# Performance work log

Hardware: AMD Instinct MI355X
Metric: run time of the kernel (lower is better)

Reference implementation:

```python
import jax, jax.numpy as jnp
import numpy as np

N = 300000; E = N - 1; A = 150000; D = 64; H = 128; T = 512
NEG_SLOPE = 0.2


def _gatv2(h, src, dst, Wl, bl, Wr, br, att, bias):
    # PyG GATv2Conv, heads=1, add_self_loops=False
    xl = h @ Wl + bl            # source transform [N,H]
    xr = h @ Wr + br            # target transform [N,H]
    e = xl[src] + xr[dst]       # [E,H]
    a = jax.nn.leaky_relu(e, NEG_SLOPE) @ att   # [E]
    amax = jax.ops.segment_max(a, dst, num_segments=N)
    ex = jnp.exp(a - amax[dst])
    denom = jax.ops.segment_sum(ex, dst, num_segments=N)
    alpha = ex / (denom[dst] + 1e-16)
    out = jax.ops.segment_sum(alpha[:, None] * xl[src], dst, num_segments=N)
    return out + bias


def setup_inputs() -> dict:
    ks = jax.random.split(jax.random.key(0), 32)
    s = 0.02
    inp = {
        'x': jax.random.normal(ks[0], (N, D), jnp.float32),
        'edge_index': jax.random.randint(ks[1], (2, E), 0, N),
        'focal_seq': jax.random.normal(ks[2], (1, D), jnp.float32),
        'child_idx': jax.random.randint(ks[3], (A,), 0, N),
        'parent_idx': jax.random.randint(ks[4], (A,), 0, N + 1) - 1,  # include -1 (no parent)
        'time_idx': jax.random.randint(ks[5], (A,), 0, T),
        'W_embed': jax.random.normal(ks[6], (D, H)) * s, 'b_embed': jnp.zeros((H,)),
        'bu_Wl': jax.random.normal(ks[7], (H, H)) * s, 'bu_bl': jnp.zeros((H,)),
        'bu_Wr': jax.random.normal(ks[8], (H, H)) * s, 'bu_br': jnp.zeros((H,)),
        'bu_att': jax.random.normal(ks[9], (H,)) * s, 'bu_bias': jnp.zeros((H,)),
        'td_Wl': jax.random.normal(ks[10], (H, H)) * s, 'td_bl': jnp.zeros((H,)),
        'td_Wr': jax.random.normal(ks[11], (H, H)) * s, 'td_br': jnp.zeros((H,)),
        'td_att': jax.random.normal(ks[12], (H,)) * s, 'td_bias': jnp.zeros((H,)),
        'time_table': jax.random.normal(ks[13], (T, H)) * s,
        'W_comb': jax.random.normal(ks[14], (2 * H, H)) * s, 'b_comb': jnp.zeros((H,)),
        'W_a1': jax.random.normal(ks[15], (3 * H, H)) * s, 'b_a1': jnp.zeros((H,)),
        'W_a2': jax.random.normal(ks[16], (H, 1)) * s, 'b_a2': jnp.zeros((1,)),
        'W_seq': jax.random.normal(ks[17], (D, H)) * s, 'b_seq': jnp.zeros((H,)),
    }
    return inp


def reference(x, edge_index, focal_seq, child_idx, parent_idx, time_idx,
              W_embed, b_embed,
              bu_Wl, bu_bl, bu_Wr, bu_br, bu_att, bu_bias,
              td_Wl, td_bl, td_Wr, td_br, td_att, td_bias,
              time_table, W_comb, b_comb, W_a1, b_a1, W_a2, b_a2,
              W_seq, b_seq):
    h = x @ W_embed + b_embed                       # [N,H]
    # bottom-up pass: edge_index flipped -> src=row1, dst=row0
    h_bu = _gatv2(h, edge_index[1], edge_index[0], bu_Wl, bu_bl, bu_Wr, bu_br, bu_att, bu_bias)
    h = h + jax.nn.relu(h_bu)
    # top-down pass: src=row0, dst=row1
    h_td = _gatv2(h, edge_index[0], edge_index[1], td_Wl, td_bl, td_Wr, td_br, td_att, td_bias)
    h = h + jax.nn.relu(h_td)
    context = focal_seq @ W_seq + b_seq             # [1,H]
    h_child = h[child_idx]                          # [A,H]
    h_parent = jnp.where((parent_idx == -1)[:, None], 0.0, h[parent_idx])
    branch = jnp.concatenate([h_child, h_parent], axis=-1) @ W_comb + b_comb  # [A,H]
    t_emb = time_table[time_idx]                    # [A,H]
    combined = jnp.concatenate([branch, t_emb, jnp.broadcast_to(context, (branch.shape[0], context.shape[1]))], axis=-1)  # [A,3H]
    logits = jax.nn.relu(combined @ W_a1 + b_a1) @ W_a2 + b_a2  # [A,1]
    return logits
```

## Files before the change

### kernel.cpp

```cpp
#include <hip/hip_runtime.h>
#include <hip/hip_bf16.h>

#define NN 300000
#define EE 299999
#define AA 150000
#define DD 64
#define HH 128
#define TT 512
#define SCAN_NB ((NN + 1023) / 1024)

typedef unsigned short u16;
typedef unsigned int u32;
typedef __attribute__((ext_vector_type(8))) short short8;
typedef __attribute__((ext_vector_type(4))) float f32x4;

__device__ __forceinline__ float bfb(u16 u) { return __uint_as_float(((u32)u) << 16); }
__device__ __forceinline__ u16 f2b(float f) {
    u32 u = __float_as_uint(f);
    u32 r = (u + 0x7FFFu + ((u >> 16) & 1u)) >> 16;
    return (u16)r;
}
__device__ __forceinline__ uint4 load8(const u16* p) { return *(const uint4*)p; }
__device__ __forceinline__ uint4 load8(const float* p) {
    float4 f1 = *(const float4*)p;
    float4 f2 = *(const float4*)(p + 4);
    union { ushort s[8]; uint4 v; } u;
    u.s[0] = f2b(f1.x); u.s[1] = f2b(f1.y); u.s[2] = f2b(f1.z); u.s[3] = f2b(f1.w);
    u.s[4] = f2b(f2.x); u.s[5] = f2b(f2.y); u.s[6] = f2b(f2.z); u.s[7] = f2b(f2.w);
    return u.v;
}
__device__ __forceinline__ void unpack8(uint4 v, float* f) {
    u32 w0 = v.x, w1 = v.y, w2 = v.z, w3 = v.w;
    f[0] = bfb((u16)w0); f[1] = bfb((u16)(w0 >> 16));
    f[2] = bfb((u16)w1); f[3] = bfb((u16)(w1 >> 16));
    f[4] = bfb((u16)w2); f[5] = bfb((u16)(w2 >> 16));
    f[6] = bfb((u16)w3); f[7] = bfb((u16)(w3 >> 16));
}
__device__ __forceinline__ int swo(int row, int kblock) {
    return row * 64 + ((kblock ^ (row & 7)) * 8);
}

__global__ __launch_bounds__(256) void k_wtrans(const float* w0, const float* w1,
                                                const float* w2, const float* w3,
                                                const float* w4, const float* w5,
                                                const float* w6, const float* w7,
                                                u16* __restrict__ wt) {
    int widx = blockIdx.x >> 3, part = blockIdx.x & 7;
    const float* W; int K = 128;
    switch (widx) {
        case 0: W = w0; break; case 1: W = w1; break;
        case 2: W = w2; break; case 3: W = w3; break;
        case 4: W = w4; break; case 5: W = w5; break;
        case 6: W = w6; break; default: W = w7; K = 64; break;
    }
    u16* dst = wt + widx * 16384;
    int total = K * 128;
    int lo = part * 2048, hi = lo + 2048;
    if (hi > total) hi = total;
    for (int idx = lo + threadIdx.x; idx < hi; idx += 256) {
        int k = idx >> 7, n = idx & 127;
        dst[n * K + k] = f2b(W[k * 128 + n]);
    }
}

__global__ void k_context(const float* __restrict__ focal, const float* __restrict__ Wseq,
                          const float* __restrict__ bseq, float* __restrict__ ctx) {
    int t = threadIdx.x;
    float acc = bseq[t];
    for (int d = 0; d < DD; ++d) acc = fmaf(focal[d], Wseq[d * HH + t], acc);
    ctx[t] = acc;
}

__global__ void k_c1(const float* __restrict__ ctx, const float* __restrict__ Wa1c,
                     const float* __restrict__ ba1, float* __restrict__ c1) {
    int t = threadIdx.x;
    float acc = ba1[t];
    for (int k = 0; k < HH; ++k) acc = fmaf(ctx[k], Wa1c[k * HH + t], acc);
    c1[t] = acc;
}

__global__ void k_tproj(const float* __restrict__ tt, const float* __restrict__ Wa1m,
                        float* __restrict__ tproj) {
    int ti = blockIdx.x, t = threadIdx.x;
    float acc = 0.f;
    for (int k = 0; k < HH; ++k)
        acc = fmaf(tt[ti * HH + k], Wa1m[k * HH + t], acc);
    tproj[(size_t)ti * HH + t] = acc;
}

__global__ void k_hist(const int* __restrict__ dst, int* __restrict__ counts) {
    int e = blockIdx.x * 256 + threadIdx.x;
    if (e < EE) atomicAdd(&counts[dst[e]], 1);
}

__global__ __launch_bounds__(256) void k_scan_block(const int* __restrict__ in,
                                                    int* __restrict__ out,
                                                    int* __restrict__ bsum, int n) {
    __shared__ int sh[256];
    int b = blockIdx.x, t = threadIdx.x;
    int base = b * 1024 + t * 4;
    int v0 = (base + 0 < n) ? in[base + 0] : 0;
    int v1 = (base + 1 < n) ? in[base + 1] : 0;
    int v2 = (base + 2 < n) ? in[base + 2] : 0;
    int v3 = (base + 3 < n) ? in[base + 3] : 0;
    int tsum = v0 + v1 + v2 + v3;
    sh[t] = tsum;
    __syncthreads();
    for (int d = 1; d < 256; d <<= 1) {
        int x = (t >= d) ? sh[t - d] : 0;
        __syncthreads();
        sh[t] += x;
        __syncthreads();
    }
    int excl = sh[t] - tsum;
    if (t == 255) bsum[b] = sh[255];
    if (base + 0 < n) out[base + 0] = excl;
    if (base + 1 < n) out[base + 1] = excl + v0;
    if (base + 2 < n) out[base + 2] = excl + v0 + v1;
    if (base + 3 < n) out[base + 3] = excl + v0 + v1 + v2;
}

__global__ __launch_bounds__(256) void k_scan_top(int* __restrict__ data, int n) {
    __shared__ int sh[256];
    int t = threadIdx.x;
    int base = t * 4;
    int v0 = (base + 0 < n) ? data[base + 0] : 0;
    int v1 = (base + 1 < n) ? data[base + 1] : 0;
    int v2 = (base + 2 < n) ? data[base + 2] : 0;
    int v3 = (base + 3 < n) ? data[base + 3] : 0;
    int tsum = v0 + v1 + v2 + v3;
    sh[t] = tsum;
    __syncthreads();
    for (int d = 1; d < 256; d <<= 1) {
        int x = (t >= d) ? sh[t - d] : 0;
        __syncthreads();
        sh[t] += x;
        __syncthreads();
    }
    int excl = sh[t] - tsum;
    if (base + 0 < n) data[base + 0] = excl;
    if (base + 1 < n) data[base + 1] = excl + v0;
    if (base + 2 < n) data[base + 2] = excl + v0 + v1;
    if (base + 3 < n) data[base + 3] = excl + v0 + v1 + v2;
}

__global__ void k_scan_add(int* __restrict__ out, const int* __restrict__ bsum, int n) {
    int i = blockIdx.x * 256 + threadIdx.x;
    if (i < n) out[i] += bsum[i >> 10];
}

__global__ void k_settail(int* o1, int* o2) {
    if (threadIdx.x == 0) { o1[NN] = EE; o2[NN] = EE; }
}

__global__ void k_scatter(const int* __restrict__ src, const int* __restrict__ dst,
                          int* __restrict__ cursor, int* __restrict__ elist) {
    int e = blockIdx.x * 256 + threadIdx.x;
    if (e >= EE) return;
    int pos = atomicAdd(&cursor[dst[e]], 1);
    elist[pos] = src[e];
}

template <int K, typename InT>
__global__ __launch_bounds__(256) void k_mfma_proj(const InT* __restrict__ in,
                                                   const u16* __restrict__ WT,
                                                   const float* __restrict__ bias,
                                                   u16* __restrict__ out, int nrows) {
    __shared__ u16 lds[17408];
    u16* a_lds = lds;
    u16* b_lds = lds + 8192;
    u16* clds = lds;
    const int t = threadIdx.x;
    const int tile_m = blockIdx.x * 128;
    const int wave = t >> 6, l = t & 15, quad = (t >> 4) & 3;
    const int wr = wave >> 1, wc = wave & 1;
    f32x4 acc[4][4] = {};

    for (int chunk = 0; chunk < K / 64; ++chunk) {
        const int c0 = chunk * 64;
        __syncthreads();
        for (int ci = t; ci < 1024; ci += 256) {
            int row = ci >> 3, kc = ci & 7;
            int grow = tile_m + row;
            uint4 v = make_uint4(0, 0, 0, 0);
            if (grow < nrows) v = load8(&in[(size_t)grow * K + c0 + kc * 8]);
            *(uint4*)&a_lds[swo(row, kc)] = v;
        }
        for (int ci = t; ci < 1024; ci += 256) {
            int n = ci >> 3, kc = ci & 7;
            *(uint4*)&b_lds[swo(n, kc)] = *(const uint4*)&WT[(size_t)n * K + c0 + kc * 8];
        }
        __syncthreads();
#pragma unroll
        for (int ks = 0; ks < 2; ++ks) {
            short8 af[4], bf[4];
#pragma unroll
            for (int i = 0; i < 4; ++i)
                af[i] = *(const short8*)&a_lds[swo(wr * 64 + i * 16 + l, ks * 4 + quad)];
#pragma unroll
            for (int j = 0; j < 4; ++j)
                bf[j] = *(const short8*)&b_lds[swo(wc * 64 + j * 16 + l, ks * 4 + quad)];
#pragma unroll
            for (int i = 0; i < 4; ++i)
#pragma unroll
                for (int j = 0; j < 4; ++j)
                    acc[i][j] = __builtin_amdgcn_mfma_f32_16x16x32_bf16(af[i], bf[j], acc[i][j], 0, 0, 0);
        }
    }
    __syncthreads();
#pragma unroll
    for (int j = 0; j < 4; ++j) {
        int col = wc * 64 + j * 16 + l;
        float b = bias[col];
#pragma unroll
        for (int i = 0; i < 4; ++i) {
            int rloc = wr * 64 + i * 16 + quad * 4;
#pragma unroll
            for (int r = 0; r < 4; ++r)
                clds[(rloc + r) * 136 + col] = f2b(acc[i][j][r] + b);
        }
    }
    __syncthreads();
#pragma unroll
    for (int it = 0; it < 8; ++it) {
        int idx = it * 256 + t;
        int row = idx >> 4, c16 = idx & 15;
        int grow = tile_m + row;
        if (grow < nrows)
            *(uint4*)&out[(size_t)grow * HH + c16 * 8] = *(const uint4*)&clds[row * 136 + c16 * 8];
    }
}

__global__ __launch_bounds__(256) void k_mfma_proj2(const u16* __restrict__ in,
                                                    const u16* __restrict__ WT1,
                                                    const u16* __restrict__ WT2,
                                                    const float* __restrict__ b1,
                                                    const float* __restrict__ b2,
                                                    u16* __restrict__ out1,
                                                    u16* __restrict__ out2, int nrows) {
    __shared__ u16 lds[24576];
    u16* a_lds = lds;
    u16* b1_lds = lds + 8192;
    u16* b2_lds = lds + 16384;
    u16* clds = lds;
    const int t = threadIdx.x;
    const int tile_m = blockIdx.x * 128;
    const int wave = t >> 6, l = t & 15, quad = (t >> 4) & 3;
    const int wr = wave >> 1, wc = wave & 1;
    f32x4 acc1[4][4] = {}, acc2[4][4] = {};

    for (int chunk = 0; chunk < 2; ++chunk) {
        const int c0 = chunk * 64;
        __syncthreads();
        for (int ci = t; ci < 1024; ci += 256) {
            int row = ci >> 3, kc = ci & 7;
            int grow = tile_m + row;
            uint4 v = make_uint4(0, 0, 0, 0);
            if (grow < nrows) v = load8(&in[(size_t)grow * HH + c0 + kc * 8]);
            *(uint4*)&a_lds[swo(row, kc)] = v;
        }
        for (int ci = t; ci < 1024; ci += 256) {
            int n = ci >> 3, kc = ci & 7;
            *(uint4*)&b1_lds[swo(n, kc)] = *(const uint4*)&WT1[(size_t)n * HH + c0 + kc * 8];
            *(uint4*)&b2_lds[swo(n, kc)] = *(const uint4*)&WT2[(size_t)n * HH + c0 + kc * 8];
        }
        __syncthreads();
#pragma unroll
        for (int ks = 0; ks < 2; ++ks) {
            short8 af[4], bf1[4], bf2[4];
#pragma unroll
            for (int i = 0; i < 4; ++i)
                af[i] = *(const short8*)&a_lds[swo(wr * 64 + i * 16 + l, ks * 4 + quad)];
#pragma unroll
            for (int j = 0; j < 4; ++j) {
                bf1[j] = *(const short8*)&b1_lds[swo(wc * 64 + j * 16 + l, ks * 4 + quad)];
                bf2[j] = *(const short8*)&b2_lds[swo(wc * 64 + j * 16 + l, ks * 4 + quad)];
            }
#pragma unroll
            for (int i = 0; i < 4; ++i)
#pragma unroll
                for (int j = 0; j < 4; ++j) {
                    acc1[i][j] = __builtin_amdgcn_mfma_f32_16x16x32_bf16(af[i], bf1[j], acc1[i][j], 0, 0, 0);
                    acc2[i][j] = __builtin_amdgcn_mfma_f32_16x16x32_bf16(af[i], bf2[j], acc2[i][j], 0, 0, 0);
                }
        }
    }
    __syncthreads();
#pragma unroll
    for (int j = 0; j < 4; ++j) {
        int col = wc * 64 + j * 16 + l;
        float b = b1[col];
#pragma unroll
        for (int i = 0; i < 4; ++i) {
            int rloc = wr * 64 + i * 16 + quad * 4;
#pragma unroll
            for (int r = 0; r < 4; ++r)
                clds[(rloc + r) * 136 + col] = f2b(acc1[i][j][r] + b);
        }
    }
    __syncthreads();
#pragma unroll
    for (int it = 0; it < 8; ++it) {
        int idx = it * 256 + t;
        int row = idx >> 4, c16 = idx & 15;
        int grow = tile_m + row;
        if (grow < nrows)
            *(uint4*)&out1[(size_t)grow * HH + c16 * 8] = *(const uint4*)&clds[row * 136 + c16 * 8];
    }
    __syncthreads();
#pragma unroll
    for (int j = 0; j < 4; ++j) {
        int col = wc * 64 + j * 16 + l;
        float b = b2[col];
#pragma unroll
        for (int i = 0; i < 4; ++i) {
            int rloc = wr * 64 + i * 16 + quad * 4;
#pragma unroll
            for (int r = 0; r < 4; ++r)
                clds[(rloc + r) * 136 + col] = f2b(acc2[i][j][r] + b);
        }
    }
    __syncthreads();
#pragma unroll
    for (int it = 0; it < 8; ++it) {
        int idx = it * 256 + t;
        int row = idx >> 4, c16 = idx & 15;
        int grow = tile_m + row;
        if (grow < nrows)
            *(uint4*)&out2[(size_t)grow * HH + c16 * 8] = *(const uint4*)&clds[row * 136 + c16 * 8];
    }
}

__global__ __launch_bounds__(256) void k_mfma_gproj(const u16* __restrict__ h,
                                                    const int* __restrict__ idx1,
                                                    const int* __restrict__ idx2,
                                                    const u16* __restrict__ WT1,
                                                    const u16* __restrict__ WT2,
                                                    const float* __restrict__ bias,
                                                    u16* __restrict__ out, int nrows) {
    __shared__ u16 lds[17408];
    u16* a_lds = lds;
    u16* b_lds = lds + 8192;
    u16* clds = lds;
    const int t = threadIdx.x;
    const int tile_m = blockIdx.x * 128;
    const int wave = t >> 6, l = t & 15, quad = (t >> 4) & 3;
    const int wr = wave >> 1, wc = wave & 1;
    f32x4 acc[4][4] = {};

    for (int pass = 0; pass < 2; ++pass) {
        const int* idx = pass ? idx2 : idx1;
        const u16* WT = pass ? WT2 : WT1;
        for (int chunk = 0; chunk < 2; ++chunk) {
            const int c0 = chunk * 64;
            __syncthreads();
            for (int ci = t; ci < 1024; ci += 256) {
                int row = ci >> 3, kc = ci & 7;
                int item = tile_m + row;
                int g = (item < nrows) ? idx[item] : -1;
                uint4 v = make_uint4(0, 0, 0, 0);
                if (g >= 0) v = load8(&h[(size_t)g * HH + c0 + kc * 8]);
                *(uint4*)&a_lds[swo(row, kc)] = v;
            }
            for (int ci = t; ci < 1024; ci += 256) {
                int n = ci >> 3, kc = ci & 7;
                *(uint4*)&b_lds[swo(n, kc)] = *(const uint4*)&WT[(size_t)n * HH + c0 + kc * 8];
            }
            __syncthreads();
#pragma unroll
            for (int ks = 0; ks < 2; ++ks) {
                short8 af[4], bf[4];
#pragma unroll
                for (int i = 0; i < 4; ++i)
                    af[i] = *(const short8*)&a_lds[swo(wr * 64 + i * 16 + l, ks * 4 + quad)];
#pragma unroll
                for (int j = 0; j < 4; ++j)
                    bf[j] = *(const short8*)&b_lds[swo(wc * 64 + j * 16 + l, ks * 4 + quad)];
#pragma unroll
                for (int i = 0; i < 4; ++i)
#pragma unroll
                    for (int j = 0; j < 4; ++j)
                        acc[i][j] = __builtin_amdgcn_mfma_f32_16x16x32_bf16(af[i], bf[j], acc[i][j], 0, 0, 0);
            }
        }
    }
    __syncthreads();
#pragma unroll
    for (int j = 0; j < 4; ++j) {
        int col = wc * 64 + j * 16 + l;
        float b = bias[col];
#pragma unroll
        for (int i = 0; i < 4; ++i) {
            int rloc = wr * 64 + i * 16 + quad * 4;
#pragma unroll
            for (int r = 0; r < 4; ++r)
                clds[(rloc + r) * 136 + col] = f2b(acc[i][j][r] + b);
        }
    }
    __syncthreads();
#pragma unroll
    for (int it = 0; it < 8; ++it) {
        int idx = it * 256 + t;
        int row = idx >> 4, c16 = idx & 15;
        int item = tile_m + row;
        if (item < nrows)
            *(uint4*)&out[(size_t)item * HH + c16 * 8] = *(const uint4*)&clds[row * 136 + c16 * 8];
    }
}

__global__ __launch_bounds__(256) void k_mfma_zlogit(const u16* __restrict__ branch,
                                                     const int* __restrict__ time_idx,
                                                     const float* __restrict__ tproj,
                                                     const float* __restrict__ c1,
                                                     const u16* __restrict__ WTa1,
                                                     const float* __restrict__ Wa2,
                                                     const float* __restrict__ ba2,
                                                     float* __restrict__ out) {
    __shared__ u16 lds[16384];
    u16* a_lds = lds;
    u16* b_lds = lds + 8192;
    __shared__ float red[2][128];
    const int t = threadIdx.x;
    const int tile_m = blockIdx.x * 128;
    const int wave = t >> 6, l = t & 15, quad = (t >> 4) & 3;
    const int wr = wave >> 1, wc = wave & 1;
    f32x4 acc[4][4] = {};

    for (int chunk = 0; chunk < 2; ++chunk) {
        const int c0 = chunk * 64;
        __syncthreads();
        for (int ci = t; ci < 1024; ci += 256) {
            int row = ci >> 3, kc = ci & 7;
            int item = tile_m + row;
            uint4 v = make_uint4(0, 0, 0, 0);
            if (item < AA) v = load8(&branch[(size_t)item * HH + c0 + kc * 8]);
            *(uint4*)&a_lds[swo(row, kc)] = v;
        }
        for (int ci = t; ci < 1024; ci += 256) {
            int n = ci >> 3, kc = ci & 7;
            *(uint4*)&b_lds[swo(n, kc)] = *(const uint4*)&WTa1[(size_t)n * HH + c0 + kc * 8];
        }
        __syncthreads();
#pragma unroll
        for (int ks = 0; ks < 2; ++ks) {
            short8 af[4], bf[4];
#pragma unroll
            for (int i = 0; i < 4; ++i)
                af[i] = *(const short8*)&a_lds[swo(wr * 64 + i * 16 + l, ks * 4 + quad)];
#pragma unroll
            for (int j = 0; j < 4; ++j)
                bf[j] = *(const short8*)&b_lds[swo(wc * 64 + j * 16 + l, ks * 4 + quad)];
#pragma unroll
            for (int i = 0; i < 4; ++i)
#pragma unroll
                for (int j = 0; j < 4; ++j)
                    acc[i][j] = __builtin_amdgcn_mfma_f32_16x16x32_bf16(af[i], bf[j], acc[i][j], 0, 0, 0);
        }
    }
    float c1v[4], wa2v[4];
#pragma unroll
    for (int j = 0; j < 4; ++j) {
        int col = wc * 64 + j * 16 + l;
        c1v[j] = c1[col];
        wa2v[j] = Wa2[col];
    }
#pragma unroll
    for (int i = 0; i < 4; ++i) {
        int rbase = tile_m + wr * 64 + i * 16 + quad * 4;
#pragma unroll
        for (int r = 0; r < 4; ++r) {
            int item = rbase + r;
            int ti = (item < AA) ? time_idx[item] : 0;
            const float* tp = tproj + (size_t)ti * HH;
            float partial = 0.f;
#pragma unroll
            for (int j = 0; j < 4; ++j) {
                int col = wc * 64 + j * 16 + l;
                float z = fmaxf(acc[i][j][r] + tp[col] + c1v[j], 0.f);
                partial = fmaf(z, wa2v[j], partial);
            }
            partial += __shfl_xor(partial, 1);
            partial += __shfl_xor(partial, 2);
            partial += __shfl_xor(partial, 4);
            partial += __shfl_xor(partial, 8);
            if (l == 0) red[wc][wr * 64 + i * 16 + quad * 4 + r] = partial;
        }
    }
    __syncthreads();
    if (t < 128) {
        int item = tile_m + t;
        if (item < AA) out[item] = red[0][t] + red[1][t] + ba2[0];
    }
}

__global__ __launch_bounds__(256) void k_gat_fused(u16* __restrict__ h,
                                                   const u16* __restrict__ xl,
                                                   const u16* __restrict__ xr,
                                                   const int* __restrict__ offs,
                                                   const int* __restrict__ elist,
                                                   const float* __restrict__ att,
                                                   const float* __restrict__ bias) {
    int g = blockIdx.x * 16 + (threadIdx.x >> 4);
    int l = threadIdx.x & 15;
    float attv[8], biasv[8];
    *(float4*)&attv[0] = *(const float4*)&att[l * 8];
    *(float4*)&attv[4] = *(const float4*)&att[l * 8 + 4];
    *(float4*)&biasv[0] = *(const float4*)&bias[l * 8];
    *(float4*)&biasv[4] = *(const float4*)&bias[l * 8 + 4];
    float xrf[8];
    unpack8(*(const uint4*)&xr[(size_t)g * HH + l * 8], xrf);
    int e0 = offs[g], e1 = offs[g + 1];

    float m = -__builtin_inff(), s = 0.f;
    float acc[8] = {};
    for (int e = e0; e < e1; ++e) {
        int sidx = elist[e];
        float xf[8];
        unpack8(*(const uint4*)&xl[(size_t)sidx * HH + l * 8], xf);
        float p = 0.f;
#pragma unroll
        for (int j = 0; j < 8; ++j) {
            float v = xf[j] + xrf[j];
            v = v >= 0.f ? v : 0.2f * v;
            p = fmaf(v, attv[j], p);
        }
        p += __shfl_xor(p, 1); p += __shfl_xor(p, 2);
        p += __shfl_xor(p, 4); p += __shfl_xor(p, 8);
        float mn = fmaxf(m, p);
        float so = __expf(m - mn);
        float w = __expf(p - mn);
        s = s * so + w;
#pragma unroll
        for (int j = 0; j < 8; ++j) acc[j] = fmaf(acc[j], so, w * xf[j]);
        m = mn;
    }
    float inv = 1.f / (s + 1e-16f);

    float hf[8];
    unpack8(*(const uint4*)&h[(size_t)g * HH + l * 8], hf);
    union { ushort sh[8]; uint4 v; } o;
#pragma unroll
    for (int j = 0; j < 8; ++j) {
        hf[j] += fmaxf(fmaf(acc[j], inv, biasv[j]), 0.f);
        o.sh[j] = f2b(hf[j]);
    }
    *(uint4*)&h[(size_t)g * HH + l * 8] = o.v;
}

typedef const float* fp;

static void build_csr(const int* src, const int* dst, int* offs, int* elist,
                      int* work, int* bsum, hipStream_t stream) {
    hipMemsetAsync(work, 0, (size_t)NN * 4, stream);
    k_hist<<<(EE + 255) / 256, 256, 0, stream>>>(dst, work);
    k_scan_block<<<SCAN_NB, 256, 0, stream>>>(work, offs, bsum, NN);
    k_scan_top<<<1, 256, 0, stream>>>(bsum, SCAN_NB);
    k_scan_add<<<(NN + 255) / 256, 256, 0, stream>>>(offs, bsum, NN);
    hipMemcpyAsync(work, offs, (size_t)NN * 4, hipMemcpyDeviceToDevice, stream);
    k_scatter<<<(EE + 255) / 256, 256, 0, stream>>>(src, dst, work, elist);
}

extern "C" void kernel_launch(void* const* d_in, const int* in_sizes, int n_in,
                              void* d_out, int out_size, void* d_ws, size_t ws_size,
                              hipStream_t stream) {
    fp x                 = (fp)d_in[0];
    const int* ei        = (const int*)d_in[1];
    fp focal             = (fp)d_in[2];
    const int* child_idx = (const int*)d_in[3];
    const int* parent_idx= (const int*)d_in[4];
    const int* time_idx  = (const int*)d_in[5];
    fp W_embed = (fp)d_in[6],  b_embed = (fp)d_in[7];
    fp bu_Wl   = (fp)d_in[8],  bu_bl   = (fp)d_in[9];
    fp bu_Wr   = (fp)d_in[10], bu_br   = (fp)d_in[11];
    fp bu_att  = (fp)d_in[12], bu_bias = (fp)d_in[13];
    fp td_Wl   = (fp)d_in[14], td_bl   = (fp)d_in[15];
    fp td_Wr   = (fp)d_in[16], td_br   = (fp)d_in[17];
    fp td_att  = (fp)d_in[18], td_bias = (fp)d_in[19];
    fp time_table = (fp)d_in[20];
    fp W_comb  = (fp)d_in[21], b_comb  = (fp)d_in[22];
    fp W_a1    = (fp)d_in[23], b_a1    = (fp)d_in[24];
    fp W_a2    = (fp)d_in[25], b_a2    = (fp)d_in[26];
    fp W_seq   = (fp)d_in[27], b_seq   = (fp)d_in[28];

    const size_t NH = (size_t)NN * HH;
    u16* wt = (u16*)d_ws;
    u16* h  = wt + 8 * 16384;
    u16* xl = h + NH;
    u16* xr = xl + NH;
    u16* branch = xl;
    float* ctx   = (float*)(xr + NH);
    float* c1v   = ctx + HH;
    float* tproj = c1v + HH;
    int* offsBU  = (int*)(tproj + (size_t)TT * HH);
    int* offsTD  = offsBU + NN + 1;
    int* elistBU = offsTD + NN + 1;
    int* elistTD = elistBU + EE;
    int* csr_work= elistTD + EE;
    int* bsum    = csr_work + NN;

    build_csr(ei + EE, ei, offsBU, elistBU, csr_work, bsum, stream);
    build_csr(ei, ei + EE, offsTD, elistTD, csr_work, bsum, stream);
    k_settail<<<1, 64, 0, stream>>>(offsBU, offsTD);

    k_wtrans<<<64, 256, 0, stream>>>(bu_Wl, bu_Wr, td_Wl, td_Wr,
                                     W_comb, W_comb + (size_t)HH * HH, W_a1, W_embed, wt);
    const u16* wt_buWl = wt + 0 * 16384;
    const u16* wt_buWr = wt + 1 * 16384;
    const u16* wt_tdWl = wt + 2 * 16384;
    const u16* wt_tdWr = wt + 3 * 16384;
    const u16* wt_combC = wt + 4 * 16384;
    const u16* wt_combP = wt + 5 * 16384;
    const u16* wt_a1   = wt + 6 * 16384;
    const u16* wt_embed = wt + 7 * 16384;

    k_context<<<1, 128, 0, stream>>>(focal, W_seq, b_seq, ctx);
    k_c1<<<1, 128, 0, stream>>>(ctx, W_a1 + (size_t)256 * HH, b_a1, c1v);
    k_tproj<<<TT, 128, 0, stream>>>(time_table, W_a1 + (size_t)128 * HH, tproj);

    const int NB = (NN + 127) / 128;
    k_mfma_proj<64, float><<<NB, 256, 0, stream>>>(x, wt_embed, b_embed, h, NN);

    k_mfma_proj2<<<NB, 256, 0, stream>>>(h, wt_buWl, wt_buWr, bu_bl, bu_br, xl, xr, NN);
    k_gat_fused<<<NN / 16, 256, 0, stream>>>(h, xl, xr, offsBU, elistBU, bu_att, bu_bias);

    k_mfma_proj2<<<NB, 256, 0, stream>>>(h, wt_tdWl, wt_tdWr, td_bl, td_br, xl, xr, NN);
    k_gat_fused<<<NN / 16, 256, 0, stream>>>(h, xl, xr, offsTD, elistTD, td_att, td_bias);

    k_mfma_gproj<<<(AA + 127) / 128, 256, 0, stream>>>(
        h, child_idx, parent_idx, wt_combC, wt_combP, b_comb, branch, AA);

    k_mfma_zlogit<<<(AA + 127) / 128, 256, 0, stream>>>(
        branch, time_idx, tproj, c1v, wt_a1, W_a2, b_a2, (float*)d_out);
}
```

Measured before the change: 632.7 us.

## Stage GEMM tiles via direct global-to-LDS loads and fuse context kernels

```diff
diff --git a/kernel.cpp b/kernel.cpp
--- a/kernel.cpp
+++ b/kernel.cpp
@@ -38,6 +38,10 @@
 }
 __device__ __forceinline__ int swo(int row, int kblock) {
     return row * 64 + ((kblock ^ (row & 7)) * 8);
+}
+__device__ __forceinline__ void gl_lds16(const u16* src, u16* ldsbase) {
+    __builtin_amdgcn_global_load_lds((const __attribute__((address_space(1))) u32*)src,
+                                     (__attribute__((address_space(3))) u32*)ldsbase, 16, 0, 0);
 }
 
 __global__ __launch_bounds__(256) void k_wtrans(const float* w0, const float* w1,
@@ -63,20 +67,18 @@
     }
 }
 
-__global__ void k_context(const float* __restrict__ focal, const float* __restrict__ Wseq,
-                          const float* __restrict__ bseq, float* __restrict__ ctx) {
+__global__ void k_ctx_c1(const float* __restrict__ focal, const float* __restrict__ Wseq,
+                         const float* __restrict__ bseq, const float* __restrict__ Wa1c,
+                         const float* __restrict__ ba1, float* __restrict__ c1) {
+    __shared__ float cs[HH];
     int t = threadIdx.x;
     float acc = bseq[t];
     for (int d = 0; d < DD; ++d) acc = fmaf(focal[d], Wseq[d * HH + t], acc);
-    ctx[t] = acc;
-}
-
-__global__ void k_c1(const float* __restrict__ ctx, const float* __restrict__ Wa1c,
-                     const float* __restrict__ ba1, float* __restrict__ c1) {
-    int t = threadIdx.x;
-    float acc = ba1[t];
-    for (int k = 0; k < HH; ++k) acc = fmaf(ctx[k], Wa1c[k * HH + t], acc);
-    c1[t] = acc;
+    cs[t] = acc;
+    __syncthreads();
+    float a2 = ba1[t];
+    for (int k = 0; k < HH; ++k) a2 = fmaf(cs[k], Wa1c[k * HH + t], a2);
+    c1[t] = a2;
 }
 
 __global__ void k_tproj(const float* __restrict__ tt, const float* __restrict__ Wa1m,
@@ -252,17 +254,16 @@
     for (int chunk = 0; chunk < 2; ++chunk) {
         const int c0 = chunk * 64;
         __syncthreads();
-        for (int ci = t; ci < 1024; ci += 256) {
-            int row = ci >> 3, kc = ci & 7;
-            int grow = tile_m + row;
-            uint4 v = make_uint4(0, 0, 0, 0);
-            if (grow < nrows) v = load8(&in[(size_t)grow * HH + c0 + kc * 8]);
-            *(uint4*)&a_lds[swo(row, kc)] = v;
-        }
-        for (int ci = t; ci < 1024; ci += 256) {
-            int n = ci >> 3, kc = ci & 7;
-            *(uint4*)&b1_lds[swo(n, kc)] = *(const uint4*)&WT1[(size_t)n * HH + c0 + kc * 8];
-            *(uint4*)&b2_lds[swo(n, kc)] = *(const uint4*)&WT2[(size_t)n * HH + c0 + kc * 8];
+#pragma unroll
+        for (int it = 0; it < 4; ++it) {
+            int ci = it * 256 + t;
+            int row = ci >> 3;
+            int colblk = ((ci & 7) ^ (row & 7)) * 8;
+            u16* wbase = lds + (ci & ~63) * 8;
+            int grow = tile_m + row; if (grow >= nrows) grow = nrows - 1;
+            gl_lds16(&in[(size_t)grow * HH + c0 + colblk], wbase);
+            gl_lds16(&WT1[(size_t)row * HH + c0 + colblk], wbase + 8192);
+            gl_lds16(&WT2[(size_t)row * HH + c0 + colblk], wbase + 16384);
         }
         __syncthreads();
 #pragma unroll
@@ -354,17 +355,27 @@
         for (int chunk = 0; chunk < 2; ++chunk) {
             const int c0 = chunk * 64;
             __syncthreads();
-            for (int ci = t; ci < 1024; ci += 256) {
-                int row = ci >> 3, kc = ci & 7;
-                int item = tile_m + row;
-                int g = (item < nrows) ? idx[item] : -1;
-                uint4 v = make_uint4(0, 0, 0, 0);
-                if (g >= 0) v = load8(&h[(size_t)g * HH + c0 + kc * 8]);
-                *(uint4*)&a_lds[swo(row, kc)] = v;
+            int gneg[4];
+#pragma unroll
+            for (int it = 0; it < 4; ++it) {
+                int ci = it * 256 + t;
+                int row = ci >> 3;
+                int colblk = ((ci & 7) ^ (row & 7)) * 8;
+                u16* wbase = lds + (ci & ~63) * 8;
+                int item = tile_m + row; if (item >= nrows) item = nrows - 1;
+                int g = idx[item];
+                gneg[it] = (g < 0);
+                if (g < 0) g = 0;
+                gl_lds16(&h[(size_t)g * HH + c0 + colblk], wbase);
+                gl_lds16(&WT[(size_t)row * HH + c0 + colblk], wbase + 8192);
             }
-            for (int ci = t; ci < 1024; ci += 256) {
-                int n = ci >> 3, kc = ci & 7;
-                *(uint4*)&b_lds[swo(n, kc)] = *(const uint4*)&WT[(size_t)n * HH + c0 + kc * 8];
+            __syncthreads();
+#pragma unroll
+            for (int it = 0; it < 4; ++it) {
+                if (gneg[it]) {
+                    int ci = it * 256 + t;
+                    *(uint4*)&a_lds[ci * 8] = make_uint4(0, 0, 0, 0);
+                }
             }
             __syncthreads();
 #pragma unroll
@@ -429,16 +440,15 @@
     for (int chunk = 0; chunk < 2; ++chunk) {
         const int c0 = chunk * 64;
         __syncthreads();
-        for (int ci = t; ci < 1024; ci += 256) {
-            int row = ci >> 3, kc = ci & 7;
-            int item = tile_m + row;
-            uint4 v = make_uint4(0, 0, 0, 0);
-            if (item < AA) v = load8(&branch[(size_t)item * HH + c0 + kc * 8]);
-            *(uint4*)&a_lds[swo(row, kc)] = v;
-        }
-        for (int ci = t; ci < 1024; ci += 256) {
-            int n = ci >> 3, kc = ci & 7;
-            *(uint4*)&b_lds[swo(n, kc)] = *(const uint4*)&WTa1[(size_t)n * HH + c0 + kc * 8];
+#pragma unroll
+        for (int it = 0; it < 4; ++it) {
+            int ci = it * 256 + t;
+            int row = ci >> 3;
+            int colblk = ((ci & 7) ^ (row & 7)) * 8;
+            u16* wbase = lds + (ci & ~63) * 8;
+            int item = tile_m + row; if (item >= AA) item = AA - 1;
+            gl_lds16(&branch[(size_t)item * HH + c0 + colblk], wbase);
+            gl_lds16(&WTa1[(size_t)row * HH + c0 + colblk], wbase + 8192);
         }
         __syncthreads();
 #pragma unroll
@@ -588,8 +598,7 @@
     u16* xl = h + NH;
     u16* xr = xl + NH;
     u16* branch = xl;
-    float* ctx   = (float*)(xr + NH);
-    float* c1v   = ctx + HH;
+    float* c1v   = (float*)(xr + NH);
     float* tproj = c1v + HH;
     int* offsBU  = (int*)(tproj + (size_t)TT * HH);
     int* offsTD  = offsBU + NN + 1;
@@ -613,8 +622,7 @@
     const u16* wt_a1   = wt + 6 * 16384;
     const u16* wt_embed = wt + 7 * 16384;
 
-    k_context<<<1, 128, 0, stream>>>(focal, W_seq, b_seq, ctx);
-    k_c1<<<1, 128, 0, stream>>>(ctx, W_a1 + (size_t)256 * HH, b_a1, c1v);
+    k_ctx_c1<<<1, 128, 0, stream>>>(focal, W_seq, b_seq, W_a1 + (size_t)256 * HH, b_a1, c1v);
     k_tproj<<<TT, 128, 0, stream>>>(time_table, W_a1 + (size_t)128 * HH, tproj);
 
     const int NB = (NN + 127) / 128;
```

Result: faster. 570.4 us (-9.8%).
